# Performance work log

Hardware: AMD Instinct MI355X
Metric: run time of the kernel (lower is better)

## Reference

```python
import jax, jax.numpy as jnp
import numpy as np

B, N, IN_DIM, DIM, NCLS = 1, 6000, 1536, 1024, 2
HEADS, DHEAD, LMK, ITERS = 8, 128, 512, 6

def _ln(x, g, b, eps=1e-5):
    mu = x.mean(-1, keepdims=True)
    v = ((x - mu) ** 2).mean(-1, keepdims=True)
    return (x - mu) * jax.lax.rsqrt(v + eps) * g + b

def _pinv(x, iters):
    # Moore-Penrose via Newton-Schulz style iteration (as in nystrom-attention)
    ax = jnp.abs(x)
    z = jnp.swapaxes(x, -1, -2) / (jnp.max(ax.sum(-1)) * jnp.max(ax.sum(-2)))
    I = jnp.eye(x.shape[-1], dtype=x.dtype)
    for _ in range(iters):
        xz = x @ z
        z = 0.25 * z @ (13.0 * I - xz @ (15.0 * I - xz @ (7.0 * I - xz)))
    return z

def _dwconv2d(x, w, b, k):
    p = k // 2
    y = jax.lax.conv_general_dilated(x, w, (1, 1), [(p, p), (p, p)],
        dimension_numbers=('NCHW', 'OIHW', 'NCHW'), feature_group_count=x.shape[1])
    return y + b[None, :, None, None]

def _nystrom(x, qkv_w, out_w, out_b, res_w):
    b, n, _ = x.shape
    pad = (LMK - n % LMK) % LMK
    xp = jnp.pad(x, ((0, 0), (pad, 0), (0, 0)))  # pad at FRONT, as in nystrom-attention
    npl = n + pad
    qkv = xp @ qkv_w.T  # [b, npl, 3*H*D]
    q, k, v = jnp.split(qkv, 3, axis=-1)
    sh = lambda t: t.reshape(b, npl, HEADS, DHEAD).transpose(0, 2, 1, 3)  # bhnd
    q, k, v = sh(q), sh(k), sh(v)
    q = q * (DHEAD ** -0.5)
    l = npl // LMK  # tokens per landmark group
    ql = q.reshape(b, HEADS, LMK, l, DHEAD).sum(3) / l
    kl = k.reshape(b, HEADS, LMK, l, DHEAD).sum(3) / l
    a1 = jax.nn.softmax(jnp.einsum('bhid,bhjd->bhij', q, kl), -1)   # [b,h,npl,LMK]
    a2 = jax.nn.softmax(jnp.einsum('bhid,bhjd->bhij', ql, kl), -1)  # [b,h,LMK,LMK]
    a3 = jnp.einsum('bhid,bhjd->bhij', ql, k)                        # [b,h,LMK,npl]
    a3 = jax.nn.softmax(a3, -1)
    out = (a1 @ _pinv(a2, ITERS)) @ (a3 @ v)
    # residual depthwise conv over sequence dim per head, kernel 33, no bias
    res = jax.lax.conv_general_dilated(v, res_w, (1, 1), [(16, 16), (0, 0)],
        dimension_numbers=('NCHW', 'OIHW', 'NCHW'), feature_group_count=HEADS)
    out = out + res
    out = out.transpose(0, 2, 1, 3).reshape(b, npl, HEADS * DHEAD)
    out = out @ out_w.T + out_b
    return out[:, -n:]

def _moe(x, w_gate, expert_w, expert_b):
    gates = jax.nn.softmax(x @ w_gate, -1)  # [B,N,3] (eval: no noise)
    eo = jax.nn.relu(jnp.einsum('bnf,eof->bneo', x, expert_w) + expert_b)  # [B,N,3,1024]
    return jnp.einsum('bne,bneo->bno', gates, eo)

def _ppeg(x, H, W, pw7, pb7, pw5, pb5, pw3, pb3):
    Bb, _, C = x.shape
    cls_tok, feat = x[:, :1], x[:, 1:]
    f = feat.transpose(0, 2, 1).reshape(Bb, C, H, W)
    f = f + _dwconv2d(f, pw7, pb7, 7) + _dwconv2d(f, pw5, pb5, 5) + _dwconv2d(f, pw3, pb3, 3)
    f = f.reshape(Bb, C, H * W).transpose(0, 2, 1)
    return jnp.concatenate([cls_tok, f], axis=1)

def setup_inputs() -> dict:
    key = jax.random.key(0)
    ks = iter(jax.random.split(key, 40))
    r = lambda *s: jax.random.normal(next(ks), s, jnp.float32) * 0.02
    inp = dict(
        data=jax.random.normal(next(ks), (B, N, IN_DIM), jnp.float32),
        w_gate=r(IN_DIM, 3),
        expert_w=r(3, DIM, IN_DIM), expert_b=r(3, DIM),
        cls_token=r(1, 1, DIM),
    )
    for i in (1, 2):
        inp[f'ln{i}_g'] = jnp.ones(DIM, jnp.float32)
        inp[f'ln{i}_b'] = jnp.zeros(DIM, jnp.float32)
        inp[f'qkv{i}_w'] = r(3 * DIM, DIM)
        inp[f'out{i}_w'] = r(DIM, DIM)
        inp[f'out{i}_b'] = r(DIM)
        inp[f'res{i}_w'] = r(HEADS, 1, 33, 1)
    for kk in (7, 5, 3):
        inp[f'pw{kk}'] = r(DIM, 1, kk, kk)
        inp[f'pb{kk}'] = r(DIM)
    inp['normf_g'] = jnp.ones(DIM, jnp.float32)
    inp['normf_b'] = jnp.zeros(DIM, jnp.float32)
    inp['fc2_w'] = r(NCLS, DIM)
    inp['fc2_b'] = r(NCLS)
    return inp

def reference(data, w_gate, expert_w, expert_b, cls_token,
              ln1_g, ln1_b, qkv1_w, out1_w, out1_b, res1_w,
              pw7, pb7, pw5, pb5, pw3, pb3,
              ln2_g, ln2_b, qkv2_w, out2_w, out2_b, res2_w,
              normf_g, normf_b, fc2_w, fc2_b):
    h = _moe(data, w_gate, expert_w, expert_b)  # [B,N,1024]
    Hn = h.shape[1]
    _H = _W = int(np.ceil(np.sqrt(Hn)))
    add = _H * _W - Hn
    h = jnp.concatenate([h, h[:, :add]], axis=1)  # square-pad by wrapping
    cls = jnp.broadcast_to(cls_token, (h.shape[0], 1, DIM))
    h = jnp.concatenate([cls, h], axis=1)  # [B, 1+HW, 1024]
    h = h + _nystrom(_ln(h, ln1_g, ln1_b), qkv1_w, out1_w, out1_b, res1_w)
    h = _ppeg(h, _H, _W, pw7, pb7, pw5, pb5, pw3, pb3)
    h = h + _nystrom(_ln(h, ln2_g, ln2_b), qkv2_w, out2_w, out2_b, res2_w)
    h0 = _ln(h, normf_g, normf_b)[:, 0]
    logits = h0 @ fc2_w.T + fc2_b
    Y_prob = jax.nn.softmax(logits, -1)
    Y_hat = jnp.argmax(logits, -1)
    return (logits, Y_prob, Y_hat)
```

## Files before the change

kernel.cpp:

```cpp
#include <hip/hip_runtime.h>
#include <hip/hip_bf16.h>

#define NTOK   6000
#define INDIM  1536
#define DIM    1024
#define NPL    6144
#define PAD    59
#define NH     6085
#define HEADS  8
#define DHEAD  128
#define LMK    512
#define LSUB   12
#define HW     78
#define QSCALE 0.08838834764831845f
#define NSPLIT 16

#define OFF_H     0LL
#define OFF_LNXO  6291456LL
#define OFF_QKVB  12582912LL
#define OFF_PBV   22020096LL
#define OFF_PM    30408704LL
#define OFF_PL    30474240LL
#define OFF_OB    30539776LL
#define OFF_VT    34603008LL
#define OFF_QL    37748736LL
#define OFF_KL    38010880LL
#define OFF_A2F   38273024LL
#define OFF_BVTB  40370176LL
#define OFF_XB    42467328LL
#define OFF_XZB   43515904LL
#define OFF_XZT7  44564480LL
#define OFF_PT15  45613056LL
#define OFF_QT13  46661632LL
#define OFF_ZB0   47710208LL
#define OFF_ZT0   48758784LL
#define OFF_ZB1   49807360LL
#define OFF_ZT1   50855936LL
#define OFF_ZBT   52428800LL
#define OFF_QWB   52690944LL
#define OFF_OWB   54263808LL
#define OFF_COLS  54788096LL
#define OFF_SCAL  54796288LL
#define OFF_DATAB 31457280LL
#define OFF_EWB   36065280LL

typedef __attribute__((ext_vector_type(8))) short s16x8;
typedef __attribute__((ext_vector_type(4))) float f32x4;

__device__ __forceinline__ ushort f2b(float f) {
    union { float f; unsigned u; } v; v.f = f;
    return (ushort)((v.u + 0x7FFF + ((v.u >> 16) & 1)) >> 16);
}
__device__ __forceinline__ float b2f(ushort h) {
    union { unsigned u; float f; } v; v.u = ((unsigned)h) << 16; return v.f;
}

__device__ __forceinline__ void gld16(const void* g, void* l) {
    __builtin_amdgcn_global_load_lds((const __attribute__((address_space(1))) void*)g,
                                     (__attribute__((address_space(3))) void*)l, 16, 0, 0);
}

__device__ __forceinline__ float blk_sum(float v) {
    __shared__ float sb[4];
    #pragma unroll
    for (int o = 32; o > 0; o >>= 1) v += __shfl_down(v, o);
    int lane = threadIdx.x & 63, w = threadIdx.x >> 6;
    __syncthreads();
    if (lane == 0) sb[w] = v;
    __syncthreads();
    return sb[0] + sb[1] + sb[2] + sb[3];
}
__device__ __forceinline__ float blk_max(float v) {
    __shared__ float sb[4];
    #pragma unroll
    for (int o = 32; o > 0; o >>= 1) v = fmaxf(v, __shfl_down(v, o));
    int lane = threadIdx.x & 63, w = threadIdx.x >> 6;
    __syncthreads();
    if (lane == 0) sb[w] = v;
    __syncthreads();
    return fmaxf(fmaxf(sb[0], sb[1]), fmaxf(sb[2], sb[3]));
}

template<int EPI>
__global__ __launch_bounds__(256)
void mg(const ushort* __restrict__ A, int lda, long long sA,
        const ushort* __restrict__ B, int ldb, long long sB,
        void* __restrict__ Cp, int ldc, long long sC,
        void* __restrict__ Tp, int ldt, long long sT,
        int M, int K, const float* __restrict__ bias,
        float alpha, float tdelta, float tsign)
{
    __shared__ ushort As[4096];
    __shared__ ushort Bs[4096];
    const int t = threadIdx.x;
    const int z = blockIdx.z;
    const ushort* Ab = A + (long long)z * sA;
    const ushort* Bb = B + (long long)z * sB;
    const int row0 = blockIdx.y * 128, col0 = blockIdx.x * 128;
    const int w = t >> 6, lane = t & 63;
    const int l4 = lane >> 2, ls = (lane & 3) * 8;
    const int q0 = w, q1 = 4 + w;
    int ar0 = row0 + q0 * 16 + l4; if (ar0 >= M) ar0 = M - 1;
    int ar1 = row0 + q1 * 16 + l4; if (ar1 >= M) ar1 = M - 1;
    const int br0 = col0 + q0 * 16 + l4;
    const int br1 = col0 + q1 * 16 + l4;
    const ushort* ap0 = Ab + (long long)ar0 * lda + ls;
    const ushort* ap1 = Ab + (long long)ar1 * lda + ls;
    const ushort* bp0 = Bb + (long long)br0 * ldb + ls;
    const ushort* bp1 = Bb + (long long)br1 * ldb + ls;
    ushort* asl0 = &As[q0 * 512];
    ushort* asl1 = &As[q1 * 512];
    ushort* bsl0 = &Bs[q0 * 512];
    ushort* bsl1 = &Bs[q1 * 512];

    const int wr = (w >> 1) * 64, wc = (w & 1) * 64;
    const int fr = lane & 15, fo = (lane >> 4) * 8;

    f32x4 acc[4][4];
    #pragma unroll
    for (int a = 0; a < 4; a++)
        #pragma unroll
        for (int b = 0; b < 4; b++)
            acc[a][b] = (f32x4){0.f, 0.f, 0.f, 0.f};

    for (int kt = 0; kt < K; kt += 32) {
        gld16(ap0 + kt, asl0);
        gld16(ap1 + kt, asl1);
        gld16(bp0 + kt, bsl0);
        gld16(bp1 + kt, bsl1);
        __syncthreads();
        s16x8 af[4], bf[4];
        #pragma unroll
        for (int a = 0; a < 4; a++) af[a] = *(const s16x8*)&As[(wr + a * 16 + fr) * 32 + fo];
        #pragma unroll
        for (int b = 0; b < 4; b++) bf[b] = *(const s16x8*)&Bs[(wc + b * 16 + fr) * 32 + fo];
        #pragma unroll
        for (int a = 0; a < 4; a++)
            #pragma unroll
            for (int b = 0; b < 4; b++)
                acc[a][b] = __builtin_amdgcn_mfma_f32_16x16x32_bf16(af[a], bf[b], acc[a][b], 0, 0, 0);
        __syncthreads();
    }

    const int er0 = row0 + wr + ((lane >> 4) << 2);
    const int ec0 = col0 + wc + fr;
    #pragma unroll
    for (int a = 0; a < 4; a++) {
        #pragma unroll
        for (int j = 0; j < 4; j++) {
            int r = er0 + a * 16 + j;
            if (r >= M) continue;
            #pragma unroll
            for (int b = 0; b < 4; b++) {
                int c = ec0 + b * 16;
                float v = alpha * acc[a][b][j];
                long long ci = z * sC + (long long)r * ldc + c;
                if constexpr (EPI == 0) ((float*)Cp)[ci] = v;
                else if constexpr (EPI == 1) ((ushort*)Cp)[ci] = f2b(c < 1024 ? v * QSCALE : v);
                else if constexpr (EPI == 2) ((ushort*)Cp)[ci] = f2b(v);
                else if constexpr (EPI == 3) ((float*)Cp)[ci] += v + bias[c];
                else {
                    ushort tv = f2b((r == c ? tdelta : 0.f) + tsign * v);
                    long long ti = z * sT + (long long)c * ldt + r;
                    if constexpr (EPI == 4) { ((ushort*)Cp)[ci] = f2b(v); ((ushort*)Tp)[ti] = tv; }
                    else { ((ushort*)Tp)[ti] = tv; }
                }
            }
        }
    }
}

template<int EPI>
__global__ __launch_bounds__(256)
void mg64(const ushort* __restrict__ A, int lda, long long sA,
          const ushort* __restrict__ B, int ldb, long long sB,
          void* __restrict__ Cp, int ldc, long long sC,
          void* __restrict__ Tp, int ldt, long long sT,
          int K, float alpha, float tdelta, float tsign)
{
    __shared__ ushort As[2048];
    __shared__ ushort Bs[4096];
    const int t = threadIdx.x;
    const int z = blockIdx.z;
    const ushort* Ab = A + (long long)z * sA;
    const ushort* Bb = B + (long long)z * sB;
    const int row0 = blockIdx.y * 64, col0 = blockIdx.x * 128;
    const int w = t >> 6, lane = t & 63;
    const int l4 = lane >> 2, ls = (lane & 3) * 8;
    const ushort* ap = Ab + (long long)(row0 + w * 16 + l4) * lda + ls;
    ushort* asl = &As[w * 16 * 32];
    const ushort* bp0 = Bb + (long long)(col0 + w * 16 + l4) * ldb + ls;
    const ushort* bp1 = Bb + (long long)(col0 + 64 + w * 16 + l4) * ldb + ls;
    ushort* bsl0 = &Bs[w * 16 * 32];
    ushort* bsl1 = &Bs[(64 + w * 16) * 32];

    const int fr = lane & 15, fo = (lane >> 4) * 8;

    f32x4 acc[4][2];
    #pragma unroll
    for (int a = 0; a < 4; a++)
        #pragma unroll
        for (int b = 0; b < 2; b++)
            acc[a][b] = (f32x4){0.f, 0.f, 0.f, 0.f};

    for (int kt = 0; kt < K; kt += 32) {
        gld16(ap + kt, asl);
        gld16(bp0 + kt, bsl0);
        gld16(bp1 + kt, bsl1);
        __syncthreads();
        s16x8 af[4], bf[2];
        #pragma unroll
        for (int a = 0; a < 4; a++) af[a] = *(const s16x8*)&As[(a * 16 + fr) * 32 + fo];
        #pragma unroll
        for (int b = 0; b < 2; b++) bf[b] = *(const s16x8*)&Bs[(w * 32 + b * 16 + fr) * 32 + fo];
        #pragma unroll
        for (int a = 0; a < 4; a++)
            #pragma unroll
            for (int b = 0; b < 2; b++)
                acc[a][b] = __builtin_amdgcn_mfma_f32_16x16x32_bf16(af[a], bf[b], acc[a][b], 0, 0, 0);
        __syncthreads();
    }

    const int er0 = row0 + ((lane >> 4) << 2);
    const int ec0 = col0 + w * 32 + fr;
    #pragma unroll
    for (int a = 0; a < 4; a++) {
        #pragma unroll
        for (int j = 0; j < 4; j++) {
            int r = er0 + a * 16 + j;
            #pragma unroll
            for (int b = 0; b < 2; b++) {
                int c = ec0 + b * 16;
                float v = alpha * acc[a][b][j];
                long long ci = z * sC + (long long)r * ldc + c;
                if constexpr (EPI == 0) ((float*)Cp)[ci] = v;
                else if constexpr (EPI == 2) ((ushort*)Cp)[ci] = f2b(v);
                else {
                    ushort tv = f2b((r == c ? tdelta : 0.f) + tsign * v);
                    long long ti = z * sT + (long long)c * ldt + r;
                    if constexpr (EPI == 4) { ((ushort*)Cp)[ci] = f2b(v); ((ushort*)Tp)[ti] = tv; }
                    else { ((ushort*)Tp)[ti] = tv; }
                }
            }
        }
    }
}

template<int MODE, int NFI>
__global__ __launch_bounds__(256)
void flash(const ushort* __restrict__ Qp, int ldq, long long sQh,
           const ushort* __restrict__ Kp, int ldk, long long sKh,
           const ushort* __restrict__ Vp, int ldv, long long sVh,
           float* __restrict__ Op, float* __restrict__ Pm, float* __restrict__ Pl,
           int nkv, int kvspan)
{
    __shared__ ushort Zs[8192];
    __shared__ ushort KPs[8192];
    ushort* Ps = KPs;
    const int t = threadIdx.x;
    const int h = blockIdx.z;
    const int q0 = blockIdx.x * (NFI * 64);
    const int kvbase = blockIdx.y * kvspan;
    const ushort* Qb = Qp + (long long)h * sQh;
    const ushort* Kb = Kp + (long long)h * sKh;
    const ushort* Vb = Vp + (long long)h * sVh;
    const int w = t >> 6, lane = t & 63;
    const int sr = lane >> 2, sc2 = (lane & 3) * 8;
    const int fr = lane & 15, fo = (lane >> 4) * 8;
    const int jr = (lane >> 4) * 4;
    const int wbase = w * (NFI * 16);

    s16x8 qr[NFI][4];
    #pragma unroll
    for (int fi = 0; fi < NFI; fi++)
        #pragma unroll
        for (int ks = 0; ks < 4; ks++)
            qr[fi][ks] = *(const s16x8*)&Qb[(long long)(q0 + wbase + fi * 16 + fr) * ldq + ks * 32 + fo];

    f32x4 oa[NFI][8];
    float mold[NFI][4], lrun[NFI][4];
    #pragma unroll
    for (int fi = 0; fi < NFI; fi++) {
        #pragma unroll
        for (int fj = 0; fj < 8; fj++) oa[fi][fj] = (f32x4){0.f,0.f,0.f,0.f};
        #pragma unroll
        for (int j = 0; j < 4; j++) { mold[fi][j] = -1e30f; lrun[fi][j] = 0.f; }
    }

    for (int c = 0; c < nkv; c++) {
        int kvp = kvbase + c * 64;
        #pragma unroll
        for (int s = 0; s < 4; s++)
            gld16(Kb + (long long)(kvp + w * 16 + sr) * ldk + s * 32 + sc2,
                  &KPs[s * 2048 + (w * 16) * 32]);
        #pragma unroll
        for (int s = 0; s < 2; s++)
            #pragma unroll
            for (int r0 = 0; r0 < 128; r0 += 64)
                gld16(Vb + (long long)(r0 + w * 16 + sr) * ldv + kvp + s * 32 + sc2,
                      &Zs[s * 4096 + (r0 + w * 16) * 32]);
        __syncthreads();

        f32x4 acc[NFI][4];
        #pragma unroll
        for (int fi = 0; fi < NFI; fi++)
            #pragma unroll
            for (int fj = 0; fj < 4; fj++) acc[fi][fj] = (f32x4){0.f,0.f,0.f,0.f};
        #pragma unroll
        for (int ks = 0; ks < 4; ks++) {
            s16x8 kb[4];
            #pragma unroll
            for (int fj = 0; fj < 4; fj++)
                kb[fj] = *(const s16x8*)&KPs[ks * 2048 + (fj * 16 + fr) * 32 + fo];
            #pragma unroll
            for (int fi = 0; fi < NFI; fi++)
                #pragma unroll
                for (int fj = 0; fj < 4; fj++)
                    acc[fi][fj] = __builtin_amdgcn_mfma_f32_16x16x32_bf16(qr[fi][ks], kb[fj], acc[fi][fj], 0, 0, 0);
        }

        float rs[NFI][4];
        #pragma unroll
        for (int fi = 0; fi < NFI; fi++) {
            #pragma unroll
            for (int j = 0; j < 4; j++) {
                float mx = acc[fi][0][j];
                #pragma unroll
                for (int fj = 1; fj < 4; fj++) mx = fmaxf(mx, acc[fi][fj][j]);
                mx = fmaxf(mx, __shfl_xor(mx, 1));
                mx = fmaxf(mx, __shfl_xor(mx, 2));
                mx = fmaxf(mx, __shfl_xor(mx, 4));
                mx = fmaxf(mx, __shfl_xor(mx, 8));
                float mn = fmaxf(mold[fi][j], mx);
                float scl = __expf(mold[fi][j] - mn);
                mold[fi][j] = mn;
                lrun[fi][j] *= scl;
                #pragma unroll
                for (int fj = 0; fj < 8; fj++) oa[fi][fj][j] *= scl;
                float r = 0.f;
                #pragma unroll
                for (int fj = 0; fj < 4; fj++) {
                    float p = __expf(acc[fi][fj][j] - mn);
                    acc[fi][fj][j] = p;
                    r += p;
                }
                r += __shfl_xor(r, 1);
                r += __shfl_xor(r, 2);
                r += __shfl_xor(r, 4);
                r += __shfl_xor(r, 8);
                rs[fi][j] = r;
            }
        }
        __syncthreads();
        #pragma unroll
        for (int fi = 0; fi < NFI; fi++)
            #pragma unroll
            for (int j = 0; j < 4; j++) {
                int row = wbase + fi * 16 + jr + j;
                lrun[fi][j] += rs[fi][j];
                #pragma unroll
                for (int fj = 0; fj < 4; fj++) {
                    int idx = (row * 64 + fj * 16 + fr) ^ ((row & 7) << 3);
                    Ps[idx] = f2b(acc[fi][fj][j]);
                }
            }
        __syncthreads();

        #pragma unroll
        for (int ks2 = 0; ks2 < 2; ks2++) {
            s16x8 pa[NFI], zb[8];
            #pragma unroll
            for (int fi = 0; fi < NFI; fi++) {
                int row = wbase + fi * 16 + fr;
                int idx = (row * 64 + ks2 * 32 + fo) ^ ((row & 7) << 3);
                pa[fi] = *(const s16x8*)&Ps[idx];
            }
            #pragma unroll
            for (int fj = 0; fj < 8; fj++)
                zb[fj] = *(const s16x8*)&Zs[ks2 * 4096 + (fj * 16 + fr) * 32 + fo];
            #pragma unroll
            for (int fi = 0; fi < NFI; fi++)
                #pragma unroll
                for (int fj = 0; fj < 8; fj++)
                    oa[fi][fj] = __builtin_amdgcn_mfma_f32_16x16x32_bf16(pa[fi], zb[fj], oa[fi][fj], 0, 0, 0);
        }
        __syncthreads();
    }

    #pragma unroll
    for (int fi = 0; fi < NFI; fi++)
        #pragma unroll
        for (int j = 0; j < 4; j++) {
            int row = wbase + fi * 16 + jr + j;
            if constexpr (MODE == 0) {
                float inv = 1.f / lrun[fi][j];
                #pragma unroll
                for (int fj = 0; fj < 8; fj++)
                    Op[(long long)(q0 + row) * DIM + h * 128 + fj * 16 + fr] = oa[fi][fj][j] * inv;
            } else {
                long long rb = (((long long)h * 512 + q0 + row) * NSPLIT + blockIdx.y) * 128;
                #pragma unroll
                for (int fj = 0; fj < 8; fj++)
                    Op[rb + fj * 16 + fr] = oa[fi][fj][j];
                if (fr == 0) {
                    long long si = ((long long)h * 512 + q0 + row) * NSPLIT + blockIdx.y;
                    Pm[si] = mold[fi][j];
                    Pl[si] = lrun[fi][j];
                }
            }
        }
}

__global__ __launch_bounds__(256)
void bv_combine(const float* __restrict__ PBV, const float* __restrict__ Pm,
                const float* __restrict__ Pl, ushort* __restrict__ BVTb)
{
    __shared__ float T[32][129];
    __shared__ float wc8[32][NSPLIT], invL[32];
    int t = threadIdx.x;
    int h = blockIdx.y, l0 = blockIdx.x * 32;
    if (t < 32) {
        long long base = ((long long)h * 512 + l0 + t) * NSPLIT;
        float m = -1e30f;
        float mv[NSPLIT], lv[NSPLIT];
        #pragma unroll
        for (int c = 0; c < NSPLIT; c++) { mv[c] = Pm[base + c]; lv[c] = Pl[base + c]; m = fmaxf(m, mv[c]); }
        float L = 0.f;
        #pragma unroll
        for (int c = 0; c < NSPLIT; c++) { float wv = __expf(mv[c] - m); wc8[t][c] = wv; L += wv * lv[c]; }
        invL[t] = 1.f / L;
    }
    __syncthreads();
    int l = t >> 3, dg = t & 7;
    long long rbase = ((long long)h * 512 + l0 + l) * NSPLIT * 128;
    #pragma unroll
    for (int dd = 0; dd < 16; dd++) {
        int d = dg * 16 + dd;
        float s = 0.f;
        #pragma unroll
        for (int c = 0; c < NSPLIT; c++) s += wc8[l][c] * PBV[rbase + c * 128 + d];
        T[l][d] = s * invL[l];
    }
    __syncthreads();
    int d = t >> 1, half = t & 1;
    #pragma unroll
    for (int lc = 0; lc < 16; lc++) {
        int l2 = half * 16 + lc;
        BVTb[(long long)h * 65536 + (long long)d * 512 + l0 + l2] = f2b(T[l2][d]);
    }
}

__global__ __launch_bounds__(256)
void cvt_bf16(const float* __restrict__ x, ushort* __restrict__ y, long long n)
{
    long long i = ((long long)blockIdx.x * 256 + threadIdx.x) * 8;
    if (i >= n) return;
    float4 a = *(const float4*)(x + i), b = *(const float4*)(x + i + 4);
    ushort4 u0 = {f2b(a.x), f2b(a.y), f2b(a.z), f2b(a.w)};
    ushort4 u1 = {f2b(b.x), f2b(b.y), f2b(b.z), f2b(b.w)};
    *(ushort4*)(y + i) = u0; *(ushort4*)(y + i + 4) = u1;
}

template<int NIT>
__global__ __launch_bounds__(256)
void softmax_rows(float* __restrict__ X, int W)
{
    long long row = blockIdx.x;
    float* x = X + row * W;
    float r[NIT];
    float m = -1e30f;
    #pragma unroll
    for (int i = 0; i < NIT; i++) { r[i] = x[threadIdx.x + i * 256]; m = fmaxf(m, r[i]); }
    m = blk_max(m);
    float s = 0.f;
    #pragma unroll
    for (int i = 0; i < NIT; i++) { r[i] = __expf(r[i] - m); s += r[i]; }
    s = blk_sum(s);
    float inv = 1.f / s;
    #pragma unroll
    for (int i = 0; i < NIT; i++) x[threadIdx.x + i * 256] = r[i] * inv;
}

__global__ __launch_bounds__(256)
void ln_pad(const float* __restrict__ H, const float* __restrict__ g,
            const float* __restrict__ b, ushort* __restrict__ X)
{
    int row = blockIdx.x, t = threadIdx.x;
    ushort* o = X + (long long)row * DIM;
    if (row < PAD) {
        #pragma unroll
        for (int i = 0; i < 4; i++) o[t + i * 256] = 0;
        return;
    }
    const float* x = H + (long long)(row - PAD) * DIM;
    float r[4]; float s = 0.f;
    #pragma unroll
    for (int i = 0; i < 4; i++) { r[i] = x[t + i * 256]; s += r[i]; }
    float mu = blk_sum(s) * (1.f / DIM);
    float v = 0.f;
    #pragma unroll
    for (int i = 0; i < 4; i++) { float d = r[i] - mu; v += d * d; }
    float var = blk_sum(v) * (1.f / DIM);
    float rs = rsqrtf(var + 1e-5f);
    #pragma unroll
    for (int i = 0; i < 4; i++) { int c = t + i * 256; o[c] = f2b((r[i] - mu) * rs * g[c] + b[c]); }
}

__global__ __launch_bounds__(128)
void landmarks(const ushort* __restrict__ QKVb, ushort* __restrict__ QL, ushort* __restrict__ KL)
{
    int L = blockIdx.x, h = blockIdx.y, d = threadIdx.x;
    float sq = 0.f, sk = 0.f;
    #pragma unroll
    for (int j = 0; j < LSUB; j++) {
        const ushort* p = QKVb + (long long)(L * LSUB + j) * 3072 + h * DHEAD + d;
        sq += b2f(p[0]);
        sk += b2f(p[1024]);
    }
    QL[(long long)(h * LMK + L) * DHEAD + d] = f2b(sq * (1.f / LSUB));
    KL[(long long)(h * LMK + L) * DHEAD + d] = f2b(sk * (1.f / LSUB));
}

__global__ void vtrans(const ushort* __restrict__ Q, ushort* __restrict__ VT)
{
    __shared__ ushort tile[32][33];
    int h = blockIdx.z, i0 = blockIdx.x * 32, d0 = blockIdx.y * 32;
    int tx = threadIdx.x, ty = threadIdx.y;
    for (int yy = ty; yy < 32; yy += 8)
        tile[yy][tx] = Q[(long long)(i0 + yy) * 3072 + 2048 + h * 128 + d0 + tx];
    __syncthreads();
    for (int yy = ty; yy < 32; yy += 8)
        VT[((long long)h * 128 + d0 + yy) * 6144 + i0 + tx] = tile[tx][yy];
}

__global__ __launch_bounds__(256)
void a2_sums2(const float* __restrict__ A2, float* __restrict__ cols)
{
    int h = blockIdx.x, slice = blockIdx.y, t = threadIdx.x;
    const float* a = A2 + (long long)h * LMK * LMK + (long long)slice * 64 * LMK;
    float s0 = 0.f, s1 = 0.f;
    #pragma unroll 4
    for (int i = 0; i < 64; i++) {
        s0 += a[(long long)i * LMK + t];
        s1 += a[(long long)i * LMK + t + 256];
    }
    atomicAdd(&cols[h * LMK + t], s0);
    atomicAdd(&cols[h * LMK + t + 256], s1);
}
__global__ __launch_bounds__(256)
void a2_scal2(const float* __restrict__ cols, float* __restrict__ scal)
{
    float mc = -1e30f;
    for (int i = threadIdx.x; i < HEADS * LMK; i += 256) mc = fmaxf(mc, cols[i]);
    mc = blk_max(mc);
    if (threadIdx.x == 0) scal[0] = 1.f / mc;
}

__global__ void z0_t(const float* __restrict__ A2, ushort* __restrict__ Xb,
                     ushort* __restrict__ Z0b, ushort* __restrict__ Z0T,
                     const float* __restrict__ scal)
{
    __shared__ float tile[32][33];
    int h = blockIdx.z;
    const float* a = A2 + (long long)h * LMK * LMK;
    float s = scal[0];
    int x0 = blockIdx.x * 32, y0 = blockIdx.y * 32;
    int tx = threadIdx.x, ty = threadIdx.y;
    long long hb = (long long)h * LMK * LMK;
    for (int yy = ty; yy < 32; yy += 8) {
        float v = a[(long long)(y0 + yy) * LMK + x0 + tx];
        tile[yy][tx] = v;
        Xb [hb + (long long)(y0 + yy) * LMK + x0 + tx] = f2b(v);
        Z0T[hb + (long long)(y0 + yy) * LMK + x0 + tx] = f2b(s * v);
    }
    __syncthreads();
    for (int yy = ty; yy < 32; yy += 8)
        Z0b[hb + (long long)(x0 + yy) * LMK + y0 + tx] = f2b(s * tile[tx][yy]);
}

__global__ __launch_bounds__(256)
void moe_combine(const float* __restrict__ X, const float* __restrict__ wg,
                 const ushort* __restrict__ EO, const float* __restrict__ eb,
                 float* __restrict__ H)
{
    int i = blockIdx.x, t = threadIdx.x;
    const float* x = X + (long long)i * INDIM;
    float g0 = 0.f, g1 = 0.f, g2 = 0.f;
    for (int f = t; f < INDIM; f += 256) {
        float xv = x[f];
        const float* w = wg + f * 3;
        g0 += xv * w[0]; g1 += xv * w[1]; g2 += xv * w[2];
    }
    g0 = blk_sum(g0); g1 = blk_sum(g1); g2 = blk_sum(g2);
    float m = fmaxf(g0, fmaxf(g1, g2));
    float e0 = __expf(g0 - m), e1 = __expf(g1 - m), e2 = __expf(g2 - m);
    float inv = 1.f / (e0 + e1 + e2);
    e0 *= inv; e1 *= inv; e2 *= inv;
    const ushort* eo = EO + (long long)i * 3072;
    for (int o = t; o < DIM; o += 256) {
        float v0 = fmaxf(b2f(eo[o])        + eb[o],        0.f);
        float v1 = fmaxf(b2f(eo[1024 + o]) + eb[1024 + o], 0.f);
        float v2 = fmaxf(b2f(eo[2048 + o]) + eb[2048 + o], 0.f);
        float r = e0 * v0 + e1 * v1 + e2 * v2;
        H[(long long)(1 + i) * DIM + o] = r;
        if (i < 84) H[(long long)(6001 + i) * DIM + o] = r;
    }
}

__global__ void cls_copy(const float* __restrict__ c, float* __restrict__ H)
{
    for (int i = threadIdx.x; i < DIM; i += 256) H[i] = c[i];
}

__global__ __launch_bounds__(256)
void resconv(const ushort* __restrict__ QKVb, const float* __restrict__ rw,
             const float* __restrict__ O, ushort* __restrict__ Ob)
{
    long long idx = (long long)blockIdx.x * 256 + threadIdx.x;
    int c = (int)(idx & 1023);
    long long i = idx >> 10;
    int h = c >> 7;
    float acc = O[idx];
    #pragma unroll
    for (int t = 0; t < 33; t++) {
        long long r = i + t - 16;
        if (r >= 0 && r < NPL) acc += rw[h * 33 + t] * b2f(QKVb[r * 3072 + 2048 + c]);
    }
    Ob[idx] = f2b(acc);
}

__global__ void h2f(const float* __restrict__ H, float* __restrict__ F)
{
    __shared__ float tile[32][33];
    int p0 = blockIdx.x * 32, c0 = blockIdx.y * 32;
    int tx = threadIdx.x, ty = threadIdx.y;
    for (int yy = ty; yy < 32; yy += 8) {
        int p = p0 + yy;
        if (p < HW * HW) tile[yy][tx] = H[(long long)(1 + p) * DIM + c0 + tx];
    }
    __syncthreads();
    for (int yy = ty; yy < 32; yy += 8) {
        int p = p0 + tx, c = c0 + yy;
        if (p < HW * HW) F[(long long)c * (HW * HW) + p] = tile[tx][yy];
    }
}
__global__ void f2h(const float* __restrict__ F2, float* __restrict__ H)
{
    __shared__ float tile[32][33];
    int c0 = blockIdx.x * 32, p0 = blockIdx.y * 32;
    int tx = threadIdx.x, ty = threadIdx.y;
    for (int yy = ty; yy < 32; yy += 8) {
        int p = p0 + tx;
        if (p < HW * HW) tile[yy][tx] = F2[(long long)(c0 + yy) * (HW * HW) + p];
    }
    __syncthreads();
    for (int yy = ty; yy < 32; yy += 8) {
        int p = p0 + yy;
        if (p < HW * HW) H[(long long)(1 + p) * DIM + c0 + tx] = tile[tx][yy];
    }
}
__global__ __launch_bounds__(256)
void ppeg_conv2(const float* __restrict__ F,
                const float* __restrict__ w7, const float* __restrict__ b7,
                const float* __restrict__ w5, const float* __restrict__ b5,
                const float* __restrict__ w3, const float* __restrict__ b3,
                float* __restrict__ F2)
{
    int c = blockIdx.x, t = threadIdx.x;
    __shared__ float plane[HW * HW];
    __shared__ float wm[49];
    for (int p = t; p < HW * HW; p += 256) plane[p] = F[(long long)c * (HW * HW) + p];
    if (t < 49) {
        int ky = t / 7 - 3, kx = t % 7 - 3;
        float w = w7[(long long)c * 49 + t];
        if (ky >= -2 && ky <= 2 && kx >= -2 && kx <= 2) w += w5[(long long)c * 25 + (ky + 2) * 5 + (kx + 2)];
        if (ky >= -1 && ky <= 1 && kx >= -1 && kx <= 1) w += w3[(long long)c * 9 + (ky + 1) * 3 + (kx + 1)];
        if (t == 24) w += 1.0f;
        wm[t] = w;
    }
    __syncthreads();
    float bsum = b7[c] + b5[c] + b3[c];
    for (int p = t; p < HW * HW; p += 256) {
        int y = p / HW, x = p - y * HW;
        float acc = bsum;
        if (y >= 3 && y < HW - 3 && x >= 3 && x < HW - 3) {
            const float* base = &plane[p];
            #pragma unroll
            for (int ky = -3; ky <= 3; ky++)
                #pragma unroll
                for (int kx = -3; kx <= 3; kx++)
                    acc += wm[(ky + 3) * 7 + kx + 3] * base[ky * HW + kx];
        } else {
            for (int ky = -3; ky <= 3; ky++) {
                int yy = y + ky; if ((unsigned)yy >= (unsigned)HW) continue;
                for (int kx = -3; kx <= 3; kx++) {
                    int xx = x + kx; if ((unsigned)xx >= (unsigned)HW) continue;
                    acc += wm[(ky + 3) * 7 + kx + 3] * plane[yy * HW + xx];
                }
            }
        }
        F2[(long long)c * (HW * HW) + p] = acc;
    }
}

__global__ __launch_bounds__(256)
void head_k(const float* __restrict__ H, const float* __restrict__ g, const float* __restrict__ b,
            const float* __restrict__ fw, const float* __restrict__ fb, float* __restrict__ out)
{
    int t = threadIdx.x;
    float r[4]; float s = 0.f;
    #pragma unroll
    for (int i = 0; i < 4; i++) { r[i] = H[t + i * 256]; s += r[i]; }
    float mu = blk_sum(s) * (1.f / DIM);
    float v = 0.f;
    #pragma unroll
    for (int i = 0; i < 4; i++) { float d = r[i] - mu; v += d * d; }
    float var = blk_sum(v) * (1.f / DIM);
    float rs = rsqrtf(var + 1e-5f);
    float d0 = 0.f, d1 = 0.f;
    #pragma unroll
    for (int i = 0; i < 4; i++) {
        int c = t + i * 256;
        float hv = (r[i] - mu) * rs * g[c] + b[c];
        d0 += hv * fw[c];
        d1 += hv * fw[DIM + c];
    }
    d0 = blk_sum(d0); d1 = blk_sum(d1);
    if (t == 0) {
        float l0 = d0 + fb[0], l1 = d1 + fb[1];
        float m = fmaxf(l0, l1);
        float e0 = __expf(l0 - m), e1 = __expf(l1 - m);
        float inv = 1.f / (e0 + e1);
        out[0] = l0; out[1] = l1;
        out[2] = e0 * inv; out[3] = e1 * inv;
        out[4] = (l1 > l0) ? 1.0f : 0.0f;
    }
}

extern "C" void kernel_launch(void* const* d_in, const int* in_sizes, int n_in,
                              void* d_out, int out_size, void* d_ws, size_t ws_size,
                              hipStream_t stream)
{
    const float* data     = (const float*)d_in[0];
    const float* w_gate   = (const float*)d_in[1];
    const float* expert_w = (const float*)d_in[2];
    const float* expert_b = (const float*)d_in[3];
    const float* cls_tok  = (const float*)d_in[4];
    const float* ln_g[2]  = {(const float*)d_in[5],  (const float*)d_in[11]};
    const float* ln_b[2]  = {(const float*)d_in[6],  (const float*)d_in[12]};
    const float* qkv_w[2] = {(const float*)d_in[7],  (const float*)d_in[13]};
    const float* out_w[2] = {(const float*)d_in[8],  (const float*)d_in[14]};
    const float* out_b[2] = {(const float*)d_in[9],  (const float*)d_in[15]};
    const float* res_w[2] = {(const float*)d_in[10], (const float*)d_in[16]};
    const float* pw7 = (const float*)d_in[17]; const float* pb7 = (const float*)d_in[18];
    const float* pw5 = (const float*)d_in[19]; const float* pb5 = (const float*)d_in[20];
    const float* pw3 = (const float*)d_in[21]; const float* pb3 = (const float*)d_in[22];
    const float* nf_g = (const float*)d_in[23]; const float* nf_b = (const float*)d_in[24];
    const float* fc2w = (const float*)d_in[25]; const float* fc2b = (const float*)d_in[26];

    float*  ws    = (float*)d_ws;
    float*  H     = ws + OFF_H;
    ushort* LNXb  = (ushort*)(ws + OFF_LNXO);
    float*  O     = ws + OFF_LNXO;
    ushort* QKVb  = (ushort*)(ws + OFF_QKVB);
    ushort* EOb   = (ushort*)(ws + OFF_QKVB);
    float*  PBV   = ws + OFF_PBV;
    float*  PM    = ws + OFF_PM;
    float*  PL    = ws + OFF_PL;
    ushort* Ob    = (ushort*)(ws + OFF_OB);
    ushort* VT    = (ushort*)(ws + OFF_VT);
    ushort* QL    = (ushort*)(ws + OFF_QL);
    ushort* KL    = (ushort*)(ws + OFF_KL);
    float*  A2F   = ws + OFF_A2F;
    ushort* BVTb  = (ushort*)(ws + OFF_BVTB);
    ushort* Xb    = (ushort*)(ws + OFF_XB);
    ushort* XZB   = (ushort*)(ws + OFF_XZB);
    ushort* XZT7  = (ushort*)(ws + OFF_XZT7);
    ushort* PT15  = (ushort*)(ws + OFF_PT15);
    ushort* QT13  = (ushort*)(ws + OFF_QT13);
    ushort* ZB[2] = {(ushort*)(ws + OFF_ZB0), (ushort*)(ws + OFF_ZB1)};
    ushort* ZT[2] = {(ushort*)(ws + OFF_ZT0), (ushort*)(ws + OFF_ZT1)};
    ushort* ZBT   = (ushort*)(ws + OFF_ZBT);
    ushort* QWB   = (ushort*)(ws + OFF_QWB);
    ushort* OWB   = (ushort*)(ws + OFF_OWB);
    ushort* DATAB = (ushort*)(ws + OFF_DATAB);
    ushort* EWB   = (ushort*)(ws + OFF_EWB);
    float*  COLS  = ws + OFF_COLS;
    float*  SCAL  = ws + OFF_SCAL;

    const long long HSB = (long long)LMK * DHEAD;
    const long long A2S = (long long)LMK * LMK;

    cvt_bf16<<<4500, 256, 0, stream>>>(data, DATAB, (long long)NTOK * INDIM);
    cvt_bf16<<<2304, 256, 0, stream>>>(expert_w, EWB, 3072LL * INDIM);
    mg<2><<<dim3(24,47,1),256,0,stream>>>(DATAB,INDIM,0, EWB,INDIM,0, EOb,3072,0,
        nullptr,0,0, NTOK,INDIM, nullptr, 1.f,0.f,0.f);
    moe_combine<<<NTOK,256,0,stream>>>(data, w_gate, EOb, expert_b, H);
    cls_copy<<<1,256,0,stream>>>(cls_tok, H);

    for (int stage = 0; stage < 2; stage++) {
        cvt_bf16<<<1536, 256, 0, stream>>>(qkv_w[stage], QWB, 3072LL * DIM);
        cvt_bf16<<<512, 256, 0, stream>>>(out_w[stage], OWB, (long long)DIM * DIM);
        ln_pad<<<NPL,256,0,stream>>>(H, ln_g[stage], ln_b[stage], LNXb);
        mg<1><<<dim3(24,48,1),256,0,stream>>>(LNXb,DIM,0, QWB,DIM,0, QKVb,3072,0,
            nullptr,0,0, NPL,DIM, nullptr, 1.f,0.f,0.f);
        landmarks<<<dim3(LMK,HEADS),128,0,stream>>>(QKVb, QL, KL);
        vtrans<<<dim3(192,4,8),dim3(32,8),0,stream>>>(QKVb, VT);
        mg64<0><<<dim3(4,8,8),256,0,stream>>>(QL,DHEAD,HSB, KL,DHEAD,HSB, A2F,LMK,A2S,
            nullptr,0,0, DHEAD, 1.f,0.f,0.f);
        softmax_rows<2><<<HEADS*LMK,256,0,stream>>>(A2F, LMK);
        hipMemsetAsync(COLS, 0, HEADS * LMK * sizeof(float), stream);
        a2_sums2<<<dim3(HEADS,8),256,0,stream>>>(A2F, COLS);
        a2_scal2<<<1,256,0,stream>>>(COLS, SCAL);
        z0_t<<<dim3(16,16,8),dim3(32,8),0,stream>>>(A2F, Xb, ZB[0], ZT[0], SCAL);
        int cur = 0;
        for (int it = 0; it < 6; it++) {
            mg64<4><<<dim3(4,8,8),256,0,stream>>>(Xb,LMK,A2S, ZT[cur],LMK,A2S, XZB,LMK,A2S,
                XZT7,LMK,A2S, LMK, 1.f, 7.f, -1.f);
            mg64<5><<<dim3(4,8,8),256,0,stream>>>(XZB,LMK,A2S, XZT7,LMK,A2S, nullptr,0,0,
                PT15,LMK,A2S, LMK, 1.f, 15.f, -1.f);
            mg64<5><<<dim3(4,8,8),256,0,stream>>>(XZB,LMK,A2S, PT15,LMK,A2S, nullptr,0,0,
                QT13,LMK,A2S, LMK, 1.f, 13.f, -1.f);
            if (it < 5)
                mg64<4><<<dim3(4,8,8),256,0,stream>>>(ZB[cur],LMK,A2S, QT13,LMK,A2S, ZB[1-cur],LMK,A2S,
                    ZT[1-cur],LMK,A2S, LMK, 0.25f, 0.f, 1.f);
            else
                mg64<2><<<dim3(4,8,8),256,0,stream>>>(ZB[cur],LMK,A2S, QT13,LMK,A2S, ZB[1-cur],LMK,A2S,
                    nullptr,0,0, LMK, 0.25f, 0.f, 1.f);
            cur = 1 - cur;
        }
        ushort* Z6 = ZB[cur];
        flash<1,2><<<dim3(4,NSPLIT,8),256,0,stream>>>(QL,DHEAD,HSB, QKVb+1024,3072,128,
            VT,NPL,(long long)DHEAD*NPL, PBV, PM, PL, 6, 384);
        bv_combine<<<dim3(16,8),256,0,stream>>>(PBV, PM, PL, BVTb);
        mg64<2><<<dim3(4,2,8),256,0,stream>>>(BVTb,LMK,HSB, Z6,LMK,A2S, ZBT,LMK,HSB,
            nullptr,0,0, LMK, 1.f,0.f,0.f);
        flash<0,1><<<dim3(96,1,8),256,0,stream>>>(QKVb,3072,128, KL,DHEAD,HSB,
            ZBT,LMK,HSB, O, nullptr, nullptr, 8, 0);
        resconv<<<(NPL*DIM)/256,256,0,stream>>>(QKVb, res_w[stage], O, Ob);
        mg<3><<<dim3(8,48,1),256,0,stream>>>(Ob + (long long)PAD*DIM,DIM,0, OWB,DIM,0, H,DIM,0,
            nullptr,0,0, NH,DIM, out_b[stage], 1.f,0.f,0.f);
        if (stage == 0) {
            float* F  = ws + OFF_QKVB;
            float* F2 = F + 6230016LL;
            h2f<<<dim3(191,32),dim3(32,8),0,stream>>>(H, F);
            ppeg_conv2<<<DIM,256,0,stream>>>(F, pw7, pb7, pw5, pb5, pw3, pb3, F2);
            f2h<<<dim3(32,191),dim3(32,8),0,stream>>>(F2, H);
        }
    }

    head_k<<<1,256,0,stream>>>(H, nf_g, nf_b, fc2w, fc2b, (float*)d_out);
}
```

Before: 1.661 ms.

## Double K-step per barrier in GEMMs and add lazy softmax rescale

Both generic GEMM kernels now stage 64 K-elements per iteration instead of 32. This halves the number of barrier pairs and gives more MFMAs per sync, at the cost of twice the LDS per block, which may reduce occupancy. The flash-style attention kernel skips the online-softmax rescale of the accumulators unless some row's max grows by more than 8, and wraps its MFMA phases in s_setprio. The lazy rescale lets exponentials run against a stale max and relies on fp32 headroom. It also assumes K is a multiple of 64.

```diff
diff --git a/kernel.cpp b/kernel.cpp
--- a/kernel.cpp
+++ b/kernel.cpp
@@ -90,8 +90,8 @@
         int M, int K, const float* __restrict__ bias,
         float alpha, float tdelta, float tsign)
 {
-    __shared__ ushort As[4096];
-    __shared__ ushort Bs[4096];
+    __shared__ ushort As[8192];
+    __shared__ ushort Bs[8192];
     const int t = threadIdx.x;
     const int z = blockIdx.z;
     const ushort* Ab = A + (long long)z * sA;
@@ -123,22 +123,29 @@
         for (int b = 0; b < 4; b++)
             acc[a][b] = (f32x4){0.f, 0.f, 0.f, 0.f};
 
-    for (int kt = 0; kt < K; kt += 32) {
+    for (int kt = 0; kt < K; kt += 64) {
         gld16(ap0 + kt, asl0);
         gld16(ap1 + kt, asl1);
         gld16(bp0 + kt, bsl0);
         gld16(bp1 + kt, bsl1);
+        gld16(ap0 + kt + 32, asl0 + 4096);
+        gld16(ap1 + kt + 32, asl1 + 4096);
+        gld16(bp0 + kt + 32, bsl0 + 4096);
+        gld16(bp1 + kt + 32, bsl1 + 4096);
         __syncthreads();
-        s16x8 af[4], bf[4];
-        #pragma unroll
-        for (int a = 0; a < 4; a++) af[a] = *(const s16x8*)&As[(wr + a * 16 + fr) * 32 + fo];
-        #pragma unroll
-        for (int b = 0; b < 4; b++) bf[b] = *(const s16x8*)&Bs[(wc + b * 16 + fr) * 32 + fo];
-        #pragma unroll
-        for (int a = 0; a < 4; a++)
-            #pragma unroll
-            for (int b = 0; b < 4; b++)
-                acc[a][b] = __builtin_amdgcn_mfma_f32_16x16x32_bf16(af[a], bf[b], acc[a][b], 0, 0, 0);
+        #pragma unroll
+        for (int half = 0; half < 2; half++) {
+            s16x8 af[4], bf[4];
+            #pragma unroll
+            for (int a = 0; a < 4; a++) af[a] = *(const s16x8*)&As[half * 4096 + (wr + a * 16 + fr) * 32 + fo];
+            #pragma unroll
+            for (int b = 0; b < 4; b++) bf[b] = *(const s16x8*)&Bs[half * 4096 + (wc + b * 16 + fr) * 32 + fo];
+            #pragma unroll
+            for (int a = 0; a < 4; a++)
+                #pragma unroll
+                for (int b = 0; b < 4; b++)
+                    acc[a][b] = __builtin_amdgcn_mfma_f32_16x16x32_bf16(af[a], bf[b], acc[a][b], 0, 0, 0);
+        }
         __syncthreads();
     }
 
@@ -178,8 +185,8 @@
           void* __restrict__ Tp, int ldt, long long sT,
           int K, float alpha, float tdelta, float tsign)
 {
-    __shared__ ushort As[2048];
-    __shared__ ushort Bs[4096];
+    __shared__ ushort As[4096];
+    __shared__ ushort Bs[8192];
     const int t = threadIdx.x;
     const int z = blockIdx.z;
     const ushort* Ab = A + (long long)z * sA;
@@ -203,21 +210,27 @@
         for (int b = 0; b < 2; b++)
             acc[a][b] = (f32x4){0.f, 0.f, 0.f, 0.f};
 
-    for (int kt = 0; kt < K; kt += 32) {
+    for (int kt = 0; kt < K; kt += 64) {
         gld16(ap + kt, asl);
         gld16(bp0 + kt, bsl0);
         gld16(bp1 + kt, bsl1);
+        gld16(ap + kt + 32, asl + 2048);
+        gld16(bp0 + kt + 32, bsl0 + 4096);
+        gld16(bp1 + kt + 32, bsl1 + 4096);
         __syncthreads();
-        s16x8 af[4], bf[2];
-        #pragma unroll
-        for (int a = 0; a < 4; a++) af[a] = *(const s16x8*)&As[(a * 16 + fr) * 32 + fo];
-        #pragma unroll
-        for (int b = 0; b < 2; b++) bf[b] = *(const s16x8*)&Bs[(w * 32 + b * 16 + fr) * 32 + fo];
-        #pragma unroll
-        for (int a = 0; a < 4; a++)
-            #pragma unroll
-            for (int b = 0; b < 2; b++)
-                acc[a][b] = __builtin_amdgcn_mfma_f32_16x16x32_bf16(af[a], bf[b], acc[a][b], 0, 0, 0);
+        #pragma unroll
+        for (int half = 0; half < 2; half++) {
+            s16x8 af[4], bf[2];
+            #pragma unroll
+            for (int a = 0; a < 4; a++) af[a] = *(const s16x8*)&As[half * 2048 + (a * 16 + fr) * 32 + fo];
+            #pragma unroll
+            for (int b = 0; b < 2; b++) bf[b] = *(const s16x8*)&Bs[half * 4096 + (w * 32 + b * 16 + fr) * 32 + fo];
+            #pragma unroll
+            for (int a = 0; a < 4; a++)
+                #pragma unroll
+                for (int b = 0; b < 2; b++)
+                    acc[a][b] = __builtin_amdgcn_mfma_f32_16x16x32_bf16(af[a], bf[b], acc[a][b], 0, 0, 0);
+        }
         __syncthreads();
     }
 
@@ -306,6 +319,7 @@
         for (int fi = 0; fi < NFI; fi++)
             #pragma unroll
             for (int fj = 0; fj < 4; fj++) acc[fi][fj] = (f32x4){0.f,0.f,0.f,0.f};
+        __builtin_amdgcn_s_setprio(1);
         #pragma unroll
         for (int ks = 0; ks < 4; ks++) {
             s16x8 kb[4];
@@ -318,29 +332,47 @@
                 for (int fj = 0; fj < 4; fj++)
                     acc[fi][fj] = __builtin_amdgcn_mfma_f32_16x16x32_bf16(qr[fi][ks], kb[fj], acc[fi][fj], 0, 0, 0);
         }
-
+        __builtin_amdgcn_s_setprio(0);
+
+        float mx[NFI][4];
+        bool need = false;
+        #pragma unroll
+        for (int fi = 0; fi < NFI; fi++) {
+            #pragma unroll
+            for (int j = 0; j < 4; j++) {
+                float m0 = acc[fi][0][j];
+                #pragma unroll
+                for (int fj = 1; fj < 4; fj++) m0 = fmaxf(m0, acc[fi][fj][j]);
+                m0 = fmaxf(m0, __shfl_xor(m0, 1));
+                m0 = fmaxf(m0, __shfl_xor(m0, 2));
+                m0 = fmaxf(m0, __shfl_xor(m0, 4));
+                m0 = fmaxf(m0, __shfl_xor(m0, 8));
+                mx[fi][j] = m0;
+                need = need || (m0 - mold[fi][j] > 8.f);
+            }
+        }
+        if (__any(need)) {
+            #pragma unroll
+            for (int fi = 0; fi < NFI; fi++)
+                #pragma unroll
+                for (int j = 0; j < 4; j++) {
+                    float mn = fmaxf(mold[fi][j], mx[fi][j]);
+                    float scl = __expf(mold[fi][j] - mn);
+                    mold[fi][j] = mn;
+                    lrun[fi][j] *= scl;
+                    #pragma unroll
+                    for (int fj = 0; fj < 8; fj++) oa[fi][fj][j] *= scl;
+                }
+        }
         float rs[NFI][4];
         #pragma unroll
         for (int fi = 0; fi < NFI; fi++) {
             #pragma unroll
             for (int j = 0; j < 4; j++) {
-                float mx = acc[fi][0][j];
-                #pragma unroll
-                for (int fj = 1; fj < 4; fj++) mx = fmaxf(mx, acc[fi][fj][j]);
-                mx = fmaxf(mx, __shfl_xor(mx, 1));
-                mx = fmaxf(mx, __shfl_xor(mx, 2));
-                mx = fmaxf(mx, __shfl_xor(mx, 4));
-                mx = fmaxf(mx, __shfl_xor(mx, 8));
-                float mn = fmaxf(mold[fi][j], mx);
-                float scl = __expf(mold[fi][j] - mn);
-                mold[fi][j] = mn;
-                lrun[fi][j] *= scl;
-                #pragma unroll
-                for (int fj = 0; fj < 8; fj++) oa[fi][fj][j] *= scl;
                 float r = 0.f;
                 #pragma unroll
                 for (int fj = 0; fj < 4; fj++) {
-                    float p = __expf(acc[fi][fj][j] - mn);
+                    float p = __expf(acc[fi][fj][j] - mold[fi][j]);
                     acc[fi][fj][j] = p;
                     r += p;
                 }
@@ -366,6 +398,7 @@
             }
         __syncthreads();
 
+        __builtin_amdgcn_s_setprio(1);
         #pragma unroll
         for (int ks2 = 0; ks2 < 2; ks2++) {
             s16x8 pa[NFI], zb[8];
@@ -384,6 +417,7 @@
                 for (int fj = 0; fj < 8; fj++)
                     oa[fi][fj] = __builtin_amdgcn_mfma_f32_16x16x32_bf16(pa[fi], zb[fj], oa[fi][fj], 0, 0, 0);
         }
+        __builtin_amdgcn_s_setprio(0);
         __syncthreads();
     }
 
```

Measured after the change: 1.564 ms. 1.06x faster.
